# Performance work log

Measured on AMD Instinct MI355X. Metric: run time of the kernel, lower is better.

## Reference

```python
import jax, jax.numpy as jnp
import numpy as np
from jax import lax

ENC_DIM, DEC_DIM, ATT_DIM, CONV_CH, KSIZE, ATT_ODIM = 1024, 1024, 512, 32, 50, 1024
SCALING = 2.0


def setup_inputs() -> dict:
    key = jax.random.key(0)
    ks = jax.random.split(key, 12)
    B, T = 32, 2000
    enc_pad = jax.random.normal(ks[0], (B, T, ENC_DIM), dtype=jnp.float32)
    enc_len = jax.random.randint(ks[1], (B,), 1000, T + 1, dtype=jnp.int32)
    dec_h = jax.random.normal(ks[2], (B, 1, DEC_DIM), dtype=jnp.float32)
    att_prev = jax.random.uniform(ks[3], (B, T), dtype=jnp.float32)
    s = 0.02
    W_enc = jax.random.normal(ks[4], (ENC_DIM, ATT_DIM), dtype=jnp.float32) * s
    b_enc = jnp.zeros((ATT_DIM,), jnp.float32)
    W_dec = jax.random.normal(ks[5], (DEC_DIM, ATT_DIM), dtype=jnp.float32) * s
    b_dec = jnp.zeros((ATT_DIM,), jnp.float32)
    W_att = jax.random.normal(ks[6], (CONV_CH, ATT_DIM), dtype=jnp.float32) * s
    b_att = jnp.zeros((ATT_DIM,), jnp.float32)
    # Conv2d(1, C, kernel=(1, 2K+1)) acting on (B,1,1,T) == 1D conv kernel (C,1,2K+1)
    conv_w = jax.random.normal(ks[7], (CONV_CH, 1, 2 * KSIZE + 1), dtype=jnp.float32) * s
    gvec = jax.random.normal(ks[8], (ATT_DIM, 1), dtype=jnp.float32) * s
    W_o = jax.random.normal(ks[9], (ENC_DIM, ATT_ODIM), dtype=jnp.float32) * s
    b_o = jnp.zeros((ATT_ODIM,), jnp.float32)
    return {"enc_pad": enc_pad, "enc_len": enc_len, "dec_h": dec_h, "att_prev": att_prev,
            "W_enc": W_enc, "b_enc": b_enc, "W_dec": W_dec, "b_dec": b_dec,
            "W_att": W_att, "b_att": b_att, "conv_w": conv_w, "gvec": gvec,
            "W_o": W_o, "b_o": b_o}


def reference(enc_pad, enc_len, dec_h, att_prev, W_enc, b_enc, W_dec, b_dec,
              W_att, b_att, conv_w, gvec, W_o, b_o):
    B, T, _ = enc_pad.shape
    enc_h = enc_pad @ W_enc + b_enc                           # [B,T,A]
    # location conv: (B,1,T) * (C,1,K) -> (B,C,T), SAME padding
    att_conv = lax.conv_general_dilated(
        att_prev[:, None, :], conv_w, window_strides=(1,),
        padding=[(KSIZE, KSIZE)], dimension_numbers=("NCH", "OIH", "NCH"))
    att_conv = jnp.transpose(att_conv, (0, 2, 1)) @ W_att + b_att  # [B,T,A]
    dec_term = (dec_h.reshape(B, DEC_DIM) @ W_dec + b_dec)[:, None, :]  # [B,1,A]
    att_state = jnp.tanh(enc_h + dec_term + att_conv)         # [B,T,A]
    e = (att_state @ gvec)[:, :, 0]                           # [B,T]
    mask = jnp.arange(T)[None, :] >= enc_len[:, None]         # True = padded
    e = jnp.where(mask, jnp.float32(-1e15), e)
    attn = jax.nn.softmax(SCALING * e, axis=1)                # [B,T]
    c = jnp.einsum("bt,btd->bd", attn, enc_pad)               # [B,enc_dim]
    c = c @ W_o + b_o                                         # [B,att_odim]
    return c, attn
```

## Files before the change

kernel.cpp:

```cpp
#include <hip/hip_runtime.h>
#include <stdint.h>
#include <stddef.h>

#define T_LEN   2000
#define BATCH   32
#define ROWS    64000
#define KDIM    1024
#define ADIM    512
#define CCH     32
#define KW      101
#define PADA    40

typedef _Float16 half8_t  __attribute__((ext_vector_type(8)));
typedef float    float4_t __attribute__((ext_vector_type(4)));

__device__ __forceinline__ half8_t pack8(float4_t a, float4_t b) {
    half8_t r;
    r[0] = (_Float16)a.x; r[1] = (_Float16)a.y;
    r[2] = (_Float16)a.z; r[3] = (_Float16)a.w;
    r[4] = (_Float16)b.x; r[5] = (_Float16)b.y;
    r[6] = (_Float16)b.z; r[7] = (_Float16)b.w;
    return r;
}

__device__ __forceinline__ float tanh_fast(float x) {
    float ax = __builtin_fabsf(x);
    ax = fminf(ax, 15.f);
    float e = __expf(2.f * ax);
    float t = 1.f - 2.f * __builtin_amdgcn_rcpf(e + 1.f);
    return (x < 0.f) ? -t : t;
}

__device__ __forceinline__ void glds16(const void* g, void* l) {
    __builtin_amdgcn_global_load_lds((const __attribute__((address_space(1))) uint32_t*)g,
                                     (__attribute__((address_space(3))) uint32_t*)l,
                                     16, 0, 0);
}

#define OFF_WENCT 0
#define OFF_WATTT 1048576
#define OFF_CONVA 1081344
#define OFF_DTERM 5177344
#define OFF_EPART 5242880
#define OFF_CPART 5498880

__global__ __launch_bounds__(256) void k_prep(const float* __restrict__ We,
                                              const float* __restrict__ Wa,
                                              const float* __restrict__ dec_h,
                                              const float* __restrict__ W_dec,
                                              const float* __restrict__ be,
                                              const float* __restrict__ bd,
                                              const float* __restrict__ ba,
                                              const float* __restrict__ att_prev,
                                              const float* __restrict__ conv_w,
                                              _Float16* __restrict__ Wet,
                                              _Float16* __restrict__ Wat,
                                              float* __restrict__ dterm,
                                              _Float16* __restrict__ convA) {
    __shared__ float smem[3460];
    const int blk = blockIdx.x, tid = threadIdx.x;

    if (blk < 512) {
        float (*tile)[33] = (float(*)[33])smem;
        const int k0 = (blk >> 4) * 32, n0 = (blk & 15) * 32;
        const int tx = tid & 31, ty = tid >> 5;
#pragma unroll
        for (int i = 0; i < 4; ++i)
            tile[ty + i * 8][tx] = We[(size_t)(k0 + ty + i * 8) * ADIM + n0 + tx];
        __syncthreads();
#pragma unroll
        for (int i = 0; i < 4; ++i)
            Wet[(size_t)(n0 + ty + i * 8) * KDIM + k0 + tx] = (_Float16)tile[tx][ty + i * 8];
    } else if (blk < 640) {
        float* dh = smem;
        float* part = smem + 1024;
        const int idx = blk - 512, b = idx >> 2, a0 = (idx & 3) * 128;
#pragma unroll
        for (int i = 0; i < 4; ++i) dh[tid + i * 256] = dec_h[b * KDIM + tid + i * 256];
        __syncthreads();
        const int a = a0 + (tid & 127), kh = (tid >> 7) * 512;
        float s = 0.f;
#pragma unroll 8
        for (int k = 0; k < 512; ++k) s += dh[kh + k] * W_dec[(size_t)(kh + k) * ADIM + a];
        part[tid] = s;
        __syncthreads();
        if (tid < 128) {
            const int aa = a0 + tid;
            dterm[b * ADIM + aa] = part[tid] + part[tid + 128] + be[aa] + bd[aa] + ba[aa];
        }
    } else if (blk < 1152) {
        float* ap = smem;
        float* w  = smem + 228;
        const int idx = blk - 640, b = idx >> 4, tt = idx & 15;
        const int t0 = tt * 128;
        for (int i = tid; i < 228; i += 256) {
            int t = t0 - 50 + i;
            ap[i] = (t >= 0 && t < T_LEN) ? att_prev[b * T_LEN + t] : 0.f;
        }
        for (int i = tid; i < CCH * KW; i += 256) w[i] = conv_w[i];
        __syncthreads();
        for (int idx2 = tid; idx2 < 128 * CCH; idx2 += 256) {
            int tl = idx2 >> 5, c = idx2 & 31;
            int t = t0 + tl;
            if (t < T_LEN) {
                float s = 0.f;
#pragma unroll
                for (int j = 0; j < KW; ++j) s += ap[tl + j] * w[c * KW + j];
                convA[(size_t)(b * T_LEN + t) * CCH + c] = (_Float16)s;
            }
        }
    } else {
#pragma unroll
        for (int rr = 0; rr < 2; ++rr) {
            const int n = tid * 2 + rr;
#pragma unroll
            for (int c = 0; c < CCH; ++c)
                Wat[n * CCH + c] = (_Float16)Wa[c * ADIM + n];
        }
    }
}

__global__ __launch_bounds__(256) void k_gemm_e(const float* __restrict__ enc,
                                                const _Float16* __restrict__ Wet,
                                                const _Float16* __restrict__ convA,
                                                const _Float16* __restrict__ Wat,
                                                const float* __restrict__ dterm,
                                                const float* __restrict__ gvec,
                                                float* __restrict__ epart) {
    __shared__ __attribute__((aligned(16))) _Float16 Ah[64 * PADA];
    __shared__ __attribute__((aligned(16))) _Float16 Bh[512 * 32];

    const int tid  = threadIdx.x;
    const int m0   = blockIdx.x * 64;
    const int wave = tid >> 6, lane = tid & 63;
    const int quad = lane >> 4, c16 = lane & 15;
    const int wn = wave * 128;

    float4_t acc[4][8];
#pragma unroll
    for (int i = 0; i < 4; ++i)
#pragma unroll
        for (int j = 0; j < 8; ++j) acc[i][j] = (float4_t){0.f, 0.f, 0.f, 0.f};

    const int arow = tid >> 2, aseg = tid & 3;
    const float* aBase = enc + (size_t)(m0 + arow) * KDIM + aseg * 8;
    const int rowl = lane >> 2, segst = lane & 3;

    float4_t pa0 = ((const float4_t*)aBase)[0];
    float4_t pa1 = ((const float4_t*)aBase)[1];

    for (int kk = 0; kk < 32; ++kk) {
        const int k0 = kk * 32;
        __syncthreads();
        *(half8_t*)&Ah[arow * PADA + aseg * 8] = pack8(pa0, pa1);
#pragma unroll
        for (int p = 0; p < 8; ++p) {
            const int nb = wn + p * 16 + rowl;
            const int segsrc = segst ^ ((nb >> 1) & 3);
            glds16(Wet + (size_t)nb * KDIM + k0 + segsrc * 8, &Bh[(wn + p * 16) * 32]);
        }
        __syncthreads();
        {
            const int kn = (kk < 31) ? (k0 + 32) : k0;
            pa0 = ((const float4_t*)(aBase + kn))[0];
            pa1 = ((const float4_t*)(aBase + kn))[1];
        }
        half8_t af[4], bf[8];
#pragma unroll
        for (int i = 0; i < 4; ++i)
            af[i] = *(const half8_t*)&Ah[(i * 16 + c16) * PADA + quad * 8];
#pragma unroll
        for (int j = 0; j < 8; ++j) {
            const int r = wn + j * 16 + c16;
            const int sb = quad ^ ((r >> 1) & 3);
            bf[j] = *(const half8_t*)&Bh[r * 32 + sb * 8];
        }
#pragma unroll
        for (int i = 0; i < 4; ++i)
#pragma unroll
            for (int j = 0; j < 8; ++j)
                acc[i][j] = __builtin_amdgcn_mfma_f32_16x16x32_f16(af[i], bf[j], acc[i][j], 0, 0, 0);
    }

    __syncthreads();
    *(half8_t*)&Ah[arow * PADA + aseg * 8] =
        *(const half8_t*)(convA + (size_t)(m0 + arow) * CCH + aseg * 8);
#pragma unroll
    for (int rr = 0; rr < 2; ++rr) {
        const int n = tid * 2 + rr;
        const int sw = (n >> 1) & 3;
#pragma unroll
        for (int s = 0; s < 4; ++s)
            *(half8_t*)&Bh[n * 32 + s * 8] = *(const half8_t*)(Wat + n * CCH + (s ^ sw) * 8);
    }
    __syncthreads();
    {
        half8_t af[4], bf[8];
#pragma unroll
        for (int i = 0; i < 4; ++i)
            af[i] = *(const half8_t*)&Ah[(i * 16 + c16) * PADA + quad * 8];
#pragma unroll
        for (int j = 0; j < 8; ++j) {
            const int r = wn + j * 16 + c16;
            const int sb = quad ^ ((r >> 1) & 3);
            bf[j] = *(const half8_t*)&Bh[r * 32 + sb * 8];
        }
#pragma unroll
        for (int i = 0; i < 4; ++i)
#pragma unroll
            for (int j = 0; j < 8; ++j)
                acc[i][j] = __builtin_amdgcn_mfma_f32_16x16x32_f16(af[i], bf[j], acc[i][j], 0, 0, 0);
    }

    float g[8], dt0[8], dt1[8];
    const int b0 = m0 / T_LEN, bt = (m0 + 63) / T_LEN;
    const int lim = (b0 + 1) * T_LEN;
#pragma unroll
    for (int j = 0; j < 8; ++j) {
        const int col = wn + j * 16 + c16;
        g[j]   = gvec[col];
        dt0[j] = dterm[b0 * ADIM + col];
        dt1[j] = dterm[bt * ADIM + col];
    }
    __syncthreads();
    float* e_lds = (float*)Ah;
#pragma unroll
    for (int i = 0; i < 4; ++i) {
#pragma unroll
        for (int r = 0; r < 4; ++r) {
            const int rl = i * 16 + quad * 4 + r;
            const bool hi = (m0 + rl) >= lim;
            float s = 0.f;
#pragma unroll
            for (int j = 0; j < 8; ++j) {
                const float dv = hi ? dt1[j] : dt0[j];
                s += tanh_fast(acc[i][j][r] + dv) * g[j];
            }
#pragma unroll
            for (int off = 1; off < 16; off <<= 1) s += __shfl_xor(s, off);
            if (c16 == 0) e_lds[rl * 4 + wave] = s;
        }
    }
    __syncthreads();
    if (tid < 64) {
        float4_t q = ((const float4_t*)e_lds)[tid];
        epart[m0 + tid] = q.x + q.y + q.z + q.w;
    }
}

__global__ __launch_bounds__(512) void k_softmax(const float* __restrict__ epart,
                                                 const int* __restrict__ enc_len,
                                                 float* __restrict__ attn) {
    __shared__ float ex[T_LEN];
    __shared__ float red[8];
    const int b = blockIdx.x, tid = threadIdx.x;
    const int len = enc_len[b];
    float lmax = -3.4e38f;
    for (int t = tid; t < T_LEN; t += 512) {
        float lg = (t < len) ? 2.f * epart[b * T_LEN + t] : -2e15f;
        ex[t] = lg;
        lmax = fmaxf(lmax, lg);
    }
    for (int off = 1; off < 64; off <<= 1) lmax = fmaxf(lmax, __shfl_xor(lmax, off));
    if ((tid & 63) == 0) red[tid >> 6] = lmax;
    __syncthreads();
    const float m = fmaxf(fmaxf(fmaxf(red[0], red[1]), fmaxf(red[2], red[3])),
                          fmaxf(fmaxf(red[4], red[5]), fmaxf(red[6], red[7])));
    float lsum = 0.f;
    for (int t = tid; t < T_LEN; t += 512) {
        float p = __expf(ex[t] - m);
        ex[t] = p;
        lsum += p;
    }
    for (int off = 1; off < 64; off <<= 1) lsum += __shfl_xor(lsum, off);
    __syncthreads();
    if ((tid & 63) == 0) red[tid >> 6] = lsum;
    __syncthreads();
    const float inv = 1.f / (red[0] + red[1] + red[2] + red[3] + red[4] + red[5] + red[6] + red[7]);
    for (int t = tid; t < T_LEN; t += 512) attn[b * T_LEN + t] = ex[t] * inv;
}

__global__ __launch_bounds__(256) void k_cpart(const float* __restrict__ attn,
                                               const float* __restrict__ enc,
                                               float* __restrict__ cpart) {
    const int b = blockIdx.y, tc = blockIdx.x, tid = threadIdx.x;
    const int t0 = tc * 125;
    float4_t s = (float4_t){0.f, 0.f, 0.f, 0.f};
    const float4_t* ep = (const float4_t*)(enc + (size_t)b * T_LEN * KDIM) + tid;
    const float* ap = attn + b * T_LEN + t0;
#pragma unroll 5
    for (int tt = 0; tt < 125; ++tt) {
        const float w = ap[tt];
        float4_t v = ep[(size_t)(t0 + tt) * 256];
        s += v * w;
    }
    *(float4_t*)&cpart[(size_t)(tc * BATCH + b) * KDIM + tid * 4] = s;
}

__global__ __launch_bounds__(256) void k_out(const float* __restrict__ cpart,
                                             const float* __restrict__ W_o,
                                             const float* __restrict__ b_o,
                                             float* __restrict__ out_c) {
    __shared__ float cm[KDIM];
    const int b = blockIdx.x, tid = threadIdx.x;
    for (int d = tid; d < KDIM; d += 256) {
        float s = 0.f;
#pragma unroll
        for (int p = 0; p < 16; ++p) s += cpart[(size_t)(p * BATCH + b) * KDIM + d];
        cm[d] = s;
    }
    __syncthreads();
    const int o = blockIdx.y * 256 + tid;
    float s = b_o[o];
#pragma unroll 8
    for (int d = 0; d < KDIM; ++d) s += cm[d] * W_o[(size_t)d * KDIM + o];
    out_c[b * KDIM + o] = s;
}

extern "C" void kernel_launch(void* const* d_in, const int* in_sizes, int n_in,
                              void* d_out, int out_size, void* d_ws, size_t ws_size,
                              hipStream_t stream) {
    const float* enc      = (const float*)d_in[0];
    const int*   enc_len  = (const int*)d_in[1];
    const float* dec_h    = (const float*)d_in[2];
    const float* att_prev = (const float*)d_in[3];
    const float* W_enc    = (const float*)d_in[4];
    const float* b_enc    = (const float*)d_in[5];
    const float* W_dec    = (const float*)d_in[6];
    const float* b_dec    = (const float*)d_in[7];
    const float* W_att    = (const float*)d_in[8];
    const float* b_att    = (const float*)d_in[9];
    const float* conv_w   = (const float*)d_in[10];
    const float* gvec     = (const float*)d_in[11];
    const float* W_o      = (const float*)d_in[12];
    const float* b_o      = (const float*)d_in[13];

    float* out_c    = (float*)d_out;
    float* out_attn = out_c + BATCH * KDIM;

    char* ws = (char*)d_ws;
    _Float16* Wet   = (_Float16*)(ws + OFF_WENCT);
    _Float16* Wat   = (_Float16*)(ws + OFF_WATTT);
    _Float16* convA = (_Float16*)(ws + OFF_CONVA);
    float*    dterm = (float*)(ws + OFF_DTERM);
    float*    epart = (float*)(ws + OFF_EPART);
    float*    cpart = (float*)(ws + OFF_CPART);

    k_prep<<<1153, 256, 0, stream>>>(W_enc, W_att, dec_h, W_dec, b_enc, b_dec, b_att,
                                     att_prev, conv_w, Wet, Wat, dterm, convA);
    k_gemm_e<<<1000, 256, 0, stream>>>(enc, Wet, convA, Wat, dterm, gvec, epart);
    k_softmax<<<BATCH, 512, 0, stream>>>(epart, enc_len, out_attn);
    k_cpart<<<dim3(16, BATCH), 256, 0, stream>>>(out_attn, enc, cpart);
    k_out<<<dim3(BATCH, 4), 256, 0, stream>>>(cpart, W_o, b_o, out_c);
}
```

Baseline: 662.2 us.

## Retile attention GEMM into 128x128 N-split blocks with double-buffered async loads

The fused enc-projection GEMM changes from 64-row blocks covering all 512 attention columns to 128x128 tiles split four ways over N. The energy partials now go to four per-column-chunk buffers that the softmax kernel sums. A and B tiles are loaded with direct global-to-LDS loads into double buffers using XOR-style rotation, and fp32 enc is packed to fp16 only at fragment-load time, which removes the register prefetch and pack-and-store of the old path. The conv features are stored as fp32 and handled as an extra K step in the same pipeline. The trade-off is that enc is read four times (once per N chunk), which relies on L2 reuse, in exchange for more blocks, higher occupancy and overlap of loads with MFMA.

```diff
diff --git a/kernel.cpp b/kernel.cpp
--- a/kernel.cpp
+++ b/kernel.cpp
@@ -9,7 +9,6 @@
 #define ADIM    512
 #define CCH     32
 #define KW      101
-#define PADA    40
 
 typedef _Float16 half8_t  __attribute__((ext_vector_type(8)));
 typedef float    float4_t __attribute__((ext_vector_type(4)));
@@ -40,9 +39,9 @@
 #define OFF_WENCT 0
 #define OFF_WATTT 1048576
 #define OFF_CONVA 1081344
-#define OFF_DTERM 5177344
-#define OFF_EPART 5242880
-#define OFF_CPART 5498880
+#define OFF_DTERM 9273344
+#define OFF_EPART 9338880
+#define OFF_CPART 10362880
 
 __global__ __launch_bounds__(256) void k_prep(const float* __restrict__ We,
                                               const float* __restrict__ Wa,
@@ -56,7 +55,7 @@
                                               _Float16* __restrict__ Wet,
                                               _Float16* __restrict__ Wat,
                                               float* __restrict__ dterm,
-                                              _Float16* __restrict__ convA) {
+                                              float* __restrict__ convA) {
     __shared__ float smem[3460];
     const int blk = blockIdx.x, tid = threadIdx.x;
 
@@ -106,7 +105,7 @@
                 float s = 0.f;
 #pragma unroll
                 for (int j = 0; j < KW; ++j) s += ap[tl + j] * w[c * KW + j];
-                convA[(size_t)(b * T_LEN + t) * CCH + c] = (_Float16)s;
+                convA[(size_t)(b * T_LEN + t) * CCH + c] = s;
             }
         }
     } else {
@@ -120,131 +119,120 @@
     }
 }
 
-__global__ __launch_bounds__(256) void k_gemm_e(const float* __restrict__ enc,
-                                                const _Float16* __restrict__ Wet,
-                                                const _Float16* __restrict__ convA,
-                                                const _Float16* __restrict__ Wat,
-                                                const float* __restrict__ dterm,
-                                                const float* __restrict__ gvec,
-                                                float* __restrict__ epart) {
-    __shared__ __attribute__((aligned(16))) _Float16 Ah[64 * PADA];
-    __shared__ __attribute__((aligned(16))) _Float16 Bh[512 * 32];
+__global__ __launch_bounds__(256, 3) void k_gemm_e(const float* __restrict__ enc,
+                                                   const _Float16* __restrict__ Wet,
+                                                   const float* __restrict__ convA,
+                                                   const _Float16* __restrict__ Wat,
+                                                   const float* __restrict__ dterm,
+                                                   const float* __restrict__ gvec,
+                                                   float* __restrict__ epart) {
+    __shared__ __attribute__((aligned(16))) float    Af[2][128 * 32];
+    __shared__ __attribute__((aligned(16))) _Float16 Bh[2][128 * 32];
 
     const int tid  = threadIdx.x;
-    const int m0   = blockIdx.x * 64;
+    const int nc   = blockIdx.x, m0 = blockIdx.y * 128, n0 = nc * 128;
     const int wave = tid >> 6, lane = tid & 63;
     const int quad = lane >> 4, c16 = lane & 15;
-    const int wn = wave * 128;
-
-    float4_t acc[4][8];
-#pragma unroll
-    for (int i = 0; i < 4; ++i)
-#pragma unroll
-        for (int j = 0; j < 8; ++j) acc[i][j] = (float4_t){0.f, 0.f, 0.f, 0.f};
-
-    const int arow = tid >> 2, aseg = tid & 3;
-    const float* aBase = enc + (size_t)(m0 + arow) * KDIM + aseg * 8;
-    const int rowl = lane >> 2, segst = lane & 3;
-
-    float4_t pa0 = ((const float4_t*)aBase)[0];
-    float4_t pa1 = ((const float4_t*)aBase)[1];
-
-    for (int kk = 0; kk < 32; ++kk) {
-        const int k0 = kk * 32;
-        __syncthreads();
-        *(half8_t*)&Ah[arow * PADA + aseg * 8] = pack8(pa0, pa1);
-#pragma unroll
-        for (int p = 0; p < 8; ++p) {
-            const int nb = wn + p * 16 + rowl;
-            const int segsrc = segst ^ ((nb >> 1) & 3);
-            glds16(Wet + (size_t)nb * KDIM + k0 + segsrc * 8, &Bh[(wn + p * 16) * 32]);
-        }
-        __syncthreads();
-        {
-            const int kn = (kk < 31) ? (k0 + 32) : k0;
-            pa0 = ((const float4_t*)(aBase + kn))[0];
-            pa1 = ((const float4_t*)(aBase + kn))[1];
-        }
-        half8_t af[4], bf[8];
-#pragma unroll
-        for (int i = 0; i < 4; ++i)
-            af[i] = *(const half8_t*)&Ah[(i * 16 + c16) * PADA + quad * 8];
-#pragma unroll
-        for (int j = 0; j < 8; ++j) {
-            const int r = wn + j * 16 + c16;
-            const int sb = quad ^ ((r >> 1) & 3);
-            bf[j] = *(const half8_t*)&Bh[r * 32 + sb * 8];
-        }
-#pragma unroll
-        for (int i = 0; i < 4; ++i)
-#pragma unroll
-            for (int j = 0; j < 8; ++j)
-                acc[i][j] = __builtin_amdgcn_mfma_f32_16x16x32_f16(af[i], bf[j], acc[i][j], 0, 0, 0);
-    }
-
-    __syncthreads();
-    *(half8_t*)&Ah[arow * PADA + aseg * 8] =
-        *(const half8_t*)(convA + (size_t)(m0 + arow) * CCH + aseg * 8);
-#pragma unroll
-    for (int rr = 0; rr < 2; ++rr) {
-        const int n = tid * 2 + rr;
-        const int sw = (n >> 1) & 3;
-#pragma unroll
-        for (int s = 0; s < 4; ++s)
-            *(half8_t*)&Bh[n * 32 + s * 8] = *(const half8_t*)(Wat + n * CCH + (s ^ sw) * 8);
-    }
-    __syncthreads();
-    {
-        half8_t af[4], bf[8];
-#pragma unroll
-        for (int i = 0; i < 4; ++i)
-            af[i] = *(const half8_t*)&Ah[(i * 16 + c16) * PADA + quad * 8];
-#pragma unroll
-        for (int j = 0; j < 8; ++j) {
-            const int r = wn + j * 16 + c16;
-            const int sb = quad ^ ((r >> 1) & 3);
-            bf[j] = *(const half8_t*)&Bh[r * 32 + sb * 8];
-        }
-#pragma unroll
-        for (int i = 0; i < 4; ++i)
-#pragma unroll
-            for (int j = 0; j < 8; ++j)
-                acc[i][j] = __builtin_amdgcn_mfma_f32_16x16x32_f16(af[i], bf[j], acc[i][j], 0, 0, 0);
-    }
-
-    float g[8], dt0[8], dt1[8];
-    const int b0 = m0 / T_LEN, bt = (m0 + 63) / T_LEN;
+    const int wm = (wave >> 1) * 64, wn = (wave & 1) * 64;
+
+    const int rlA = lane >> 3, segA = lane & 7;
+    const int rlB = lane >> 2, segB = lane & 3;
+    const int aOff = ((segA - rlA) & 7) * 4;
+    const int bOff = ((segB - ((rlB >> 1) & 3)) & 3) * 8;
+
+    const float*    aG = enc + (size_t)(m0 + wave * 32 + rlA) * KDIM + aOff;
+    const _Float16* bG = Wet + (size_t)(n0 + wave * 32 + rlB) * KDIM + bOff;
+    const float*    aC = convA + (size_t)(m0 + wave * 32 + rlA) * CCH + aOff;
+    const _Float16* bC = Wat + (size_t)(n0 + wave * 32 + rlB) * CCH + bOff;
+
+    const int aR0 = ((c16 + quad * 2 + 0) & 7) * 4;
+    const int aR1 = ((c16 + quad * 2 + 1) & 7) * 4;
+    const int bR  = ((quad + (c16 >> 1)) & 3) * 8;
+
+    float g[4], dt0[4], dt1[4];
+    const int b0 = m0 / T_LEN, b1 = (m0 + 127) / T_LEN;
     const int lim = (b0 + 1) * T_LEN;
 #pragma unroll
-    for (int j = 0; j < 8; ++j) {
-        const int col = wn + j * 16 + c16;
+    for (int j = 0; j < 4; ++j) {
+        const int col = n0 + wn + j * 16 + c16;
         g[j]   = gvec[col];
         dt0[j] = dterm[b0 * ADIM + col];
-        dt1[j] = dterm[bt * ADIM + col];
-    }
-    __syncthreads();
-    float* e_lds = (float*)Ah;
+        dt1[j] = dterm[b1 * ADIM + col];
+    }
+
+    float4_t acc[4][4];
+#pragma unroll
+    for (int i = 0; i < 4; ++i)
+#pragma unroll
+        for (int j = 0; j < 4; ++j) acc[i][j] = (float4_t){0.f, 0.f, 0.f, 0.f};
+
+#pragma unroll
+    for (int i = 0; i < 4; ++i)
+        glds16(aG + (size_t)i * 8 * KDIM, &Af[0][(wave * 32 + i * 8) * 32]);
+#pragma unroll
+    for (int i = 0; i < 2; ++i)
+        glds16(bG + (size_t)i * 16 * KDIM, &Bh[0][(wave * 32 + i * 16) * 32]);
+    __syncthreads();
+
+    for (int kk = 0; kk < 33; ++kk) {
+        const int cur = kk & 1, nxt = cur ^ 1;
+        if (kk < 32) {
+            if (kk + 1 < 32) {
+                const int kn = (kk + 1) * 32;
+#pragma unroll
+                for (int i = 0; i < 4; ++i)
+                    glds16(aG + (size_t)i * 8 * KDIM + kn, &Af[nxt][(wave * 32 + i * 8) * 32]);
+#pragma unroll
+                for (int i = 0; i < 2; ++i)
+                    glds16(bG + (size_t)i * 16 * KDIM + kn, &Bh[nxt][(wave * 32 + i * 16) * 32]);
+            } else {
+#pragma unroll
+                for (int i = 0; i < 4; ++i)
+                    glds16(aC + (size_t)i * 8 * CCH, &Af[nxt][(wave * 32 + i * 8) * 32]);
+#pragma unroll
+                for (int i = 0; i < 2; ++i)
+                    glds16(bC + (size_t)i * 16 * CCH, &Bh[nxt][(wave * 32 + i * 16) * 32]);
+            }
+        }
+        half8_t af[4], bf[4];
+#pragma unroll
+        for (int i = 0; i < 4; ++i) {
+            const float* base = &Af[cur][(wm + i * 16 + c16) * 32];
+            float4_t u0 = *(const float4_t*)(base + aR0);
+            float4_t u1 = *(const float4_t*)(base + aR1);
+            af[i] = pack8(u0, u1);
+        }
+#pragma unroll
+        for (int j = 0; j < 4; ++j)
+            bf[j] = *(const half8_t*)&Bh[cur][(wn + j * 16 + c16) * 32 + bR];
+#pragma unroll
+        for (int i = 0; i < 4; ++i)
+#pragma unroll
+            for (int j = 0; j < 4; ++j)
+                acc[i][j] = __builtin_amdgcn_mfma_f32_16x16x32_f16(af[i], bf[j], acc[i][j], 0, 0, 0);
+        __syncthreads();
+    }
+
+    float* e_lds = (float*)&Bh[0][0];
 #pragma unroll
     for (int i = 0; i < 4; ++i) {
 #pragma unroll
         for (int r = 0; r < 4; ++r) {
-            const int rl = i * 16 + quad * 4 + r;
-            const bool hi = (m0 + rl) >= lim;
+            const int rloc = wm + i * 16 + quad * 4 + r;
+            const bool hi = (m0 + rloc) >= lim;
             float s = 0.f;
 #pragma unroll
-            for (int j = 0; j < 8; ++j) {
-                const float dv = hi ? dt1[j] : dt0[j];
-                s += tanh_fast(acc[i][j][r] + dv) * g[j];
-            }
+            for (int j = 0; j < 4; ++j)
+                s += tanh_fast(acc[i][j][r] + (hi ? dt1[j] : dt0[j])) * g[j];
 #pragma unroll
             for (int off = 1; off < 16; off <<= 1) s += __shfl_xor(s, off);
-            if (c16 == 0) e_lds[rl * 4 + wave] = s;
-        }
-    }
-    __syncthreads();
-    if (tid < 64) {
-        float4_t q = ((const float4_t*)e_lds)[tid];
-        epart[m0 + tid] = q.x + q.y + q.z + q.w;
+            if (c16 == 0) e_lds[rloc * 2 + (wave & 1)] = s;
+        }
+    }
+    __syncthreads();
+    if (tid < 128) {
+        const float2 q = ((const float2*)e_lds)[tid];
+        epart[nc * ROWS + m0 + tid] = q.x + q.y;
     }
 }
 
@@ -257,7 +245,9 @@
     const int len = enc_len[b];
     float lmax = -3.4e38f;
     for (int t = tid; t < T_LEN; t += 512) {
-        float lg = (t < len) ? 2.f * epart[b * T_LEN + t] : -2e15f;
+        float e = epart[b * T_LEN + t] + epart[ROWS + b * T_LEN + t]
+                + epart[2 * ROWS + b * T_LEN + t] + epart[3 * ROWS + b * T_LEN + t];
+        float lg = (t < len) ? 2.f * e : -2e15f;
         ex[t] = lg;
         lmax = fmaxf(lmax, lg);
     }
@@ -339,16 +329,16 @@
     float* out_attn = out_c + BATCH * KDIM;
 
     char* ws = (char*)d_ws;
-    _Float16* Wet   = (_Float16*)(ws + OFF_WENCT);
-    _Float16* Wat   = (_Float16*)(ws + OFF_WATTT);
-    _Float16* convA = (_Float16*)(ws + OFF_CONVA);
-    float*    dterm = (float*)(ws + OFF_DTERM);
-    float*    epart = (float*)(ws + OFF_EPART);
-    float*    cpart = (float*)(ws + OFF_CPART);
+    _Float16* Wet    = (_Float16*)(ws + OFF_WENCT);
+    _Float16* Wat    = (_Float16*)(ws + OFF_WATTT);
+    float*    convAF = (float*)(ws + OFF_CONVA);
+    float*    dterm  = (float*)(ws + OFF_DTERM);
+    float*    epart  = (float*)(ws + OFF_EPART);
+    float*    cpart  = (float*)(ws + OFF_CPART);
 
     k_prep<<<1153, 256, 0, stream>>>(W_enc, W_att, dec_h, W_dec, b_enc, b_dec, b_att,
-                                     att_prev, conv_w, Wet, Wat, dterm, convA);
-    k_gemm_e<<<1000, 256, 0, stream>>>(enc, Wet, convA, Wat, dterm, gvec, epart);
+                                     att_prev, conv_w, Wet, Wat, dterm, convAF);
+    k_gemm_e<<<dim3(4, 500), 256, 0, stream>>>(enc, Wet, convAF, Wat, dterm, gvec, epart);
     k_softmax<<<BATCH, 512, 0, stream>>>(epart, enc_len, out_attn);
     k_cpart<<<dim3(16, BATCH), 256, 0, stream>>>(out_attn, enc, cpart);
     k_out<<<dim3(BATCH, 4), 256, 0, stream>>>(cpart, W_o, b_o, out_c);
```

New measurement: 657.6 us. Within noise of the previous version (-0.7%).
